# Kernel tuning notes

Measured on AMD Instinct MI355X. Metric: run time of the kernel, lower is better.

## Reference

```python
import jax, jax.numpy as jnp
import numpy as np

B, S, H, NCOL, NH = 32, 512, 768, 32, 12
HD = H // NH  # head dim 64
LN_EPS = 1e-12


def setup_inputs() -> dict:
    key = jax.random.key(0)
    ks = jax.random.split(key, 20)
    s = 0.02
    inp = {
        'hidden_states': jax.random.normal(ks[0], (B, S, H), jnp.float32),
        'column_embeddings': jax.random.normal(ks[1], (B, NCOL, H), jnp.float32),
        'column_categories': jax.random.randint(ks[2], (B, NCOL), 0, 2, jnp.int32),
        'value_mask': jax.random.randint(ks[3], (B, S), 0, NCOL + 1, jnp.int32),
        'Wd': jax.random.normal(ks[4], (H, H), jnp.float32) * s,
        'bd': jnp.zeros((H,), jnp.float32),
        'Wc': jax.random.normal(ks[5], (H, H), jnp.float32) * s,
        'bc': jnp.zeros((H,), jnp.float32),
        'Wq': jax.random.normal(ks[6], (H, H), jnp.float32) * s,
        'bq': jnp.zeros((H,), jnp.float32),
        'Wk': jax.random.normal(ks[7], (H, H), jnp.float32) * s,
        'bk': jnp.zeros((H,), jnp.float32),
        'Wv': jax.random.normal(ks[8], (H, H), jnp.float32) * s,
        'bv': jnp.zeros((H,), jnp.float32),
        'Wo': jax.random.normal(ks[9], (H, H), jnp.float32) * s,
        'bo': jnp.zeros((H,), jnp.float32),
        'ln_g': jnp.ones((H,), jnp.float32),
        'ln_b': jnp.zeros((H,), jnp.float32),
    }
    return inp


def _layernorm(x, g, b):
    mu = jnp.mean(x, axis=-1, keepdims=True)
    var = jnp.mean(jnp.square(x - mu), axis=-1, keepdims=True)
    return (x - mu) * jax.lax.rsqrt(var + LN_EPS) * g + b


def reference(hidden_states, column_embeddings, column_categories, value_mask,
              Wd, bd, Wc, bc, Wq, bq, Wk, bk, Wv, bv, Wo, bo, ln_g, ln_b):
    # dense branch
    h_ = hidden_states @ Wd.T + bd  # [B,S,H]
    # column gather: zero out category==0 columns, prepend zero row for index 0
    table = column_embeddings * (column_categories == 1)[..., None].astype(column_embeddings.dtype)
    table = jnp.concatenate([jnp.zeros_like(table[:, :1]), table], axis=1)  # [B,NCOL+1,H]
    h_col = jnp.take_along_axis(table, value_mask[..., None].astype(jnp.int32), axis=1)  # [B,S,H]
    h = jax.nn.gelu(h_ + (h_col @ Wc.T + bc), approximate=False)
    # Roberta self-attention
    def heads(x):
        return x.reshape(B, S, NH, HD).transpose(0, 2, 1, 3)  # [B,NH,S,HD]
    q = heads(h @ Wq.T + bq)
    k = heads(h @ Wk.T + bk)
    v = heads(h @ Wv.T + bv)
    scores = jnp.einsum('bhsd,bhtd->bhst', q, k) / jnp.sqrt(jnp.float32(HD))
    probs = jax.nn.softmax(scores, axis=-1)
    ctx = jnp.einsum('bhst,bhtd->bhsd', probs, v).transpose(0, 2, 1, 3).reshape(B, S, H)
    # self-output: dense + residual + layernorm
    out = _layernorm(ctx @ Wo.T + bo + h, ln_g, ln_b)
    return out
```

## Files before the change

kernel.cpp:

```cpp
#include <hip/hip_runtime.h>
#include <hip/hip_bf16.h>
#include <math.h>
#include <stdint.h>

#define B_    32
#define S_    512
#define H_    768
#define NH_   12
#define HD_   64
#define NCOL_ 32
#define M_    (B_*S_)

typedef __bf16 bf16;
typedef __bf16 bf16x8 __attribute__((ext_vector_type(8)));
typedef __bf16 bf16x4 __attribute__((ext_vector_type(4)));
typedef float  f32x4  __attribute__((ext_vector_type(4)));

__device__ __forceinline__ void async_load16(const void* g, void* l) {
    __builtin_amdgcn_global_load_lds(
        (__attribute__((address_space(1))) unsigned int*)g,
        (__attribute__((address_space(3))) unsigned int*)l, 16, 0, 0);
}

__device__ __forceinline__ bf16x8 cvt8(const float* p) {
    const float4* fp = (const float4*)p;
    float4 x = fp[0], y = fp[1];
    bf16x8 r;
    r[0] = (bf16)x.x; r[1] = (bf16)x.y; r[2] = (bf16)x.z; r[3] = (bf16)x.w;
    r[4] = (bf16)y.x; r[5] = (bf16)y.y; r[6] = (bf16)y.z; r[7] = (bf16)y.w;
    return r;
}

__global__ __launch_bounds__(256) void cvt_kernel(
    const float* __restrict__ hidden, const float* __restrict__ ce,
    const int* __restrict__ cc, const int* __restrict__ vm,
    const float* __restrict__ Wd, const float* __restrict__ Wc,
    const float* __restrict__ Wq, const float* __restrict__ Wk,
    const float* __restrict__ Wv, const float* __restrict__ Wo,
    const float* __restrict__ bq, const float* __restrict__ bk,
    const float* __restrict__ bv,
    bf16* __restrict__ hbf, bf16* __restrict__ hcol,
    bf16* __restrict__ wpack, float* __restrict__ bqkv)
{
    int blk = blockIdx.x;
    if (blk < 6144) {
        int id = blk * 256 + threadIdx.x;
        int row = id / 96, c = id - row * 96;
        *(bf16x8*)&hbf[(long)row * H_ + c * 8] = cvt8(hidden + (long)row * H_ + c * 8);
    } else if (blk < 12288) {
        int id = (blk - 6144) * 256 + threadIdx.x;
        int row = id / 96, c = id - row * 96;
        int b = row >> 9;
        int m = vm[row];
        bf16x8 val;
#pragma unroll
        for (int i = 0; i < 8; i++) val[i] = (bf16)0.0f;
        if (m > 0) {
            int col = m - 1;
            if (cc[b * NCOL_ + col] == 1)
                val = cvt8(ce + ((long)(b * NCOL_ + col)) * H_ + c * 8);
        }
        *(bf16x8*)&hcol[(long)row * H_ + c * 8] = val;
    } else {
        int id = (blk - 12288) * 256 + threadIdx.x;
        if (id < 442368) {
            const float* src;
            int r = id;
            if      (r < 73728)  { src = Wd; }
            else if (r < 147456) { src = Wc; r -= 73728; }
            else if (r < 221184) { src = Wq; r -= 147456; }
            else if (r < 294912) { src = Wk; r -= 221184; }
            else if (r < 368640) { src = Wv; r -= 294912; }
            else                 { src = Wo; r -= 368640; }
            *(bf16x8*)&wpack[(long)id * 8] = cvt8(src + (long)r * 8);
        } else if (id < 442656) {
            int j0 = (id - 442368) * 8;
#pragma unroll
            for (int i = 0; i < 8; i++) {
                int j = j0 + i;
                float v = (j < 768) ? bq[j] : (j < 1536) ? bk[j - 768] : bv[j - 1536];
                bqkv[j] = v;
            }
        }
    }
}

__global__ __launch_bounds__(512, 4) void gemm_qkv(
    const bf16* __restrict__ A, const bf16* __restrict__ Bw,
    const float* __restrict__ bias, bf16* __restrict__ out)
{
    __shared__ __align__(16) bf16 LB[36864];

    const int tid  = threadIdx.x;
    const int lane = tid & 63;
    const int wave = tid >> 6;
    const int wr   = wave >> 1;
    const int wc   = wave & 1;
    const int quad = lane >> 4;
    const int ln16 = lane & 15;

    const int bid = blockIdx.x;
    const int xcd = bid & 7;
    const int idx = bid >> 3;
    const int m0  = (xcd * 8 + (idx & 7)) * 256;
    const int n0  = (idx >> 3) * 128;

    int arow[2], acol[2];
#pragma unroll
    for (int q = 0; q < 2; q++) {
        int l = q * 512 + tid;
        int row = l >> 2;
        arow[q] = row;
        acol[q] = ((l & 3) ^ ((row >> 1) & 3)) * 8;
    }
    const int brow = tid >> 2;
    const int bcol = ((tid & 3) ^ ((brow >> 1) & 3)) * 8;

    auto stage = [&](int kt, int bsel) {
        int kk = kt * 32;
        const bf16* ag = A + kk;
        const bf16* bg = Bw + kk;
        bf16* SAb = &LB[bsel * 8192];
        bf16* SBb = &LB[24576 + bsel * 4096];
        async_load16(ag + (long)(m0 + arow[0]) * H_ + acol[0], SAb + tid * 8);
        async_load16(ag + (long)(m0 + arow[1]) * H_ + acol[1], SAb + 4096 + tid * 8);
        async_load16(bg + (long)(n0 + brow)    * H_ + bcol,    SBb + tid * 8);
    };

    f32x4 acc[4][4];
    const f32x4 zero4 = {0.f, 0.f, 0.f, 0.f};
#pragma unroll
    for (int i = 0; i < 4; i++)
#pragma unroll
        for (int j = 0; j < 4; j++) acc[i][j] = zero4;

    const int s4 = (ln16 >> 1) & 3;
    int aoff[4], boff[4];
#pragma unroll
    for (int i = 0; i < 4; i++) {
        aoff[i] = (wr * 64 + i * 16 + ln16) * 32 + (quad ^ s4) * 8;
        boff[i] = (wc * 64 + i * 16 + ln16) * 32 + (quad ^ s4) * 8;
    }

    const int nt = 24;

    stage(0, 0);
    stage(1, 1);
    asm volatile("s_waitcnt vmcnt(3)" ::: "memory");
    __builtin_amdgcn_sched_barrier(0);
    __builtin_amdgcn_s_barrier();

    int bs = 0;
    for (int t = 0; t < nt; ++t) {
        const int ps = (bs + 2 >= 3) ? bs - 1 : bs + 2;

        bf16x8 af[4], bfr[4];
#pragma unroll
        for (int i = 0; i < 4; i++) af[i]  = *(const bf16x8*)&LB[bs * 8192 + aoff[i]];
#pragma unroll
        for (int j = 0; j < 4; j++) bfr[j] = *(const bf16x8*)&LB[24576 + bs * 4096 + boff[j]];
        if (t + 2 < nt) stage(t + 2, ps);

        __builtin_amdgcn_s_setprio(1);
#pragma unroll
        for (int i = 0; i < 4; i++)
#pragma unroll
            for (int j = 0; j < 4; j++)
                acc[i][j] = __builtin_amdgcn_mfma_f32_16x16x32_bf16(af[i], bfr[j], acc[i][j], 0, 0, 0);
        __builtin_amdgcn_s_setprio(0);

        if (t + 2 < nt)       { asm volatile("s_waitcnt vmcnt(3)" ::: "memory"); }
        else if (t + 1 < nt)  { asm volatile("s_waitcnt vmcnt(0)" ::: "memory"); }
        __builtin_amdgcn_sched_barrier(0);
        if (t + 1 < nt) __builtin_amdgcn_s_barrier();
        bs = (bs + 1 == 3) ? 0 : bs + 1;
    }

    __syncthreads();
    bf16* scr = &LB[wave * 4608];

    const int cs0  = n0 + wc * 64;
    const int sec  = (cs0 >= 1536) ? 2 : ((cs0 >= 768) ? 1 : 0);
    const int head = (cs0 - sec * 768) >> 6;
    bf16* dst = out + (long)sec * M_ * H_;

#pragma unroll
    for (int j = 0; j < 4; j++) {
        const int d_loc = j * 16 + ln16;
        const float bj = bias[cs0 + d_loc];
#pragma unroll
        for (int i = 0; i < 4; i++) {
#pragma unroll
            for (int r = 0; r < 4; r++) {
                const int s_loc = i * 16 + quad * 4 + r;
                const float v = acc[i][j][r] + bj;
                scr[(sec == 2) ? (d_loc * 72 + s_loc) : (s_loc * 72 + d_loc)] = (bf16)v;
            }
        }
    }
    asm volatile("s_waitcnt lgkmcnt(0)" ::: "memory");
    __builtin_amdgcn_sched_barrier(0);

    const int g8 = lane >> 3;
    const int o8 = (lane & 7) * 8;
    if (sec < 2) {
#pragma unroll
        for (int it = 0; it < 8; it++) {
            const int s_loc = it * 8 + g8;
            const int row_s = m0 + wr * 64 + s_loc;
            const int b = row_s >> 9, s = row_s & 511;
            *(bf16x8*)&dst[(((long)(b * NH_ + head)) * S_ + s) * HD_ + o8] =
                *(const bf16x8*)&scr[s_loc * 72 + o8];
        }
    } else {
        const int row0 = m0 + wr * 64;
        const int b = row0 >> 9, sb = row0 & 511;
#pragma unroll
        for (int it = 0; it < 8; it++) {
            const int d_loc = it * 8 + g8;
            *(bf16x8*)&dst[(((long)(b * NH_ + head)) * HD_ + d_loc) * S_ + sb + o8] =
                *(const bf16x8*)&scr[d_loc * 72 + o8];
        }
    }
}

template<int MODE>
__global__ __launch_bounds__(256, 3) void gemm_bt(
    const bf16* __restrict__ A0, const bf16* __restrict__ A1,
    const bf16* __restrict__ B0, const bf16* __restrict__ B1,
    const float* __restrict__ bias1, const float* __restrict__ bias2,
    const bf16* __restrict__ resid, bf16* __restrict__ out,
    int K, int KSPLIT)
{
    __shared__ __align__(16) bf16 SA[3][128 * 32];
    __shared__ __align__(16) bf16 SB[3][128 * 32];

    const int tid  = threadIdx.x;
    const int lane = tid & 63;
    const int wave = tid >> 6;
    const int wr   = wave >> 1;
    const int wc   = wave & 1;
    const int quad = lane >> 4;
    const int ln16 = lane & 15;

    const int bid = blockIdx.x;
    const int xcd = bid & 7;
    const int idx = bid >> 3;
    const int m0  = (xcd * 16 + (idx & 15)) * 128;
    const int n0  = (idx >> 4) * 128;

    int arow[2], acol[2];
#pragma unroll
    for (int q = 0; q < 2; q++) {
        int l = q * 256 + tid;
        int row = l >> 2;
        arow[q] = row;
        acol[q] = ((l & 3) ^ ((row >> 1) & 3)) * 8;
    }

    auto stage = [&](int kt, int bsel) {
        int kk = kt * 32;
        const bf16* ag = (kk < KSPLIT) ? A0 + kk : A1 + (kk - KSPLIT);
        const bf16* bg = (kk < KSPLIT) ? B0 + kk : B1 + (kk - KSPLIT);
        async_load16(ag + (long)(m0 + arow[0]) * H_ + acol[0], &SA[bsel][tid * 8]);
        async_load16(ag + (long)(m0 + arow[1]) * H_ + acol[1], &SA[bsel][2048 + tid * 8]);
        async_load16(bg + (long)(n0 + arow[0]) * H_ + acol[0], &SB[bsel][tid * 8]);
        async_load16(bg + (long)(n0 + arow[1]) * H_ + acol[1], &SB[bsel][2048 + tid * 8]);
    };

    f32x4 acc[4][4];
    const f32x4 zero4 = {0.f, 0.f, 0.f, 0.f};
#pragma unroll
    for (int i = 0; i < 4; i++)
#pragma unroll
        for (int j = 0; j < 4; j++) acc[i][j] = zero4;

    const int s4 = (ln16 >> 1) & 3;
    int aoff[4], boff[4];
#pragma unroll
    for (int i = 0; i < 4; i++) {
        aoff[i] = (wr * 64 + i * 16 + ln16) * 32 + (quad ^ s4) * 8;
        boff[i] = (wc * 64 + i * 16 + ln16) * 32 + (quad ^ s4) * 8;
    }

    const int nt = K >> 5;

    stage(0, 0);
    stage(1, 1);
    asm volatile("s_waitcnt vmcnt(4)" ::: "memory");
    __builtin_amdgcn_sched_barrier(0);
    __builtin_amdgcn_s_barrier();

    int bs = 0;
    for (int t = 0; t < nt; ++t) {
        const int ps = (bs + 2 >= 3) ? bs - 1 : bs + 2;

        bf16x8 af[4], bfr[4];
#pragma unroll
        for (int i = 0; i < 4; i++) af[i]  = *(const bf16x8*)&SA[bs][aoff[i]];
#pragma unroll
        for (int j = 0; j < 4; j++) bfr[j] = *(const bf16x8*)&SB[bs][boff[j]];
        if (t + 2 < nt) stage(t + 2, ps);

        __builtin_amdgcn_s_setprio(1);
#pragma unroll
        for (int i = 0; i < 4; i++)
#pragma unroll
            for (int j = 0; j < 4; j++)
                acc[i][j] = __builtin_amdgcn_mfma_f32_16x16x32_bf16(af[i], bfr[j], acc[i][j], 0, 0, 0);
        __builtin_amdgcn_s_setprio(0);

        if (t + 2 < nt)       { asm volatile("s_waitcnt vmcnt(4)" ::: "memory"); }
        else if (t + 1 < nt)  { asm volatile("s_waitcnt vmcnt(0)" ::: "memory"); }
        __builtin_amdgcn_sched_barrier(0);
        if (t + 1 < nt) __builtin_amdgcn_s_barrier();
        bs = (bs + 1 == 3) ? 0 : bs + 1;
    }

    const int c_r = quad * 4;
    const int c_c = ln16;

#pragma unroll
    for (int j = 0; j < 4; j++) {
        const int col = n0 + wc * 64 + j * 16 + c_c;
        float bias = bias1[col];
        if (MODE == 0) bias += bias2[col];
#pragma unroll
        for (int i = 0; i < 4; i++) {
#pragma unroll
            for (int r = 0; r < 4; r++) {
                const int row = m0 + wr * 64 + i * 16 + c_r + r;
                float v = acc[i][j][r] + bias;
                if (MODE == 0) {
                    v = 0.5f * v * (1.0f + erff(v * 0.70710678118654752f));
                    out[(long)row * H_ + col] = (bf16)v;
                } else {
                    v += (float)resid[(long)row * H_ + col];
                    out[(long)row * H_ + col] = (bf16)v;
                }
            }
        }
    }
}

#define QP 72

__global__ __launch_bounds__(256) void attn_kernel(
    const bf16* __restrict__ q, const bf16* __restrict__ k,
    const bf16* __restrict__ vt, bf16* __restrict__ ctx)
{
    __shared__ __align__(16) bf16 Qs[64 * QP];
    __shared__ __align__(16) bf16 Ks[64 * QP];
    __shared__ __align__(16) bf16 Vt[64 * QP];
    __shared__ __align__(16) bf16 Ps[4][16 * QP];

    const int tid  = threadIdx.x;
    const int lane = tid & 63;
    const int w    = tid >> 6;
    const int quad = lane >> 4;
    const int ln16 = lane & 15;

    const int bid = blockIdx.x;
    const int qt  = bid / 384;
    const int g   = bid - qt * 384;
    const int b   = g / 12;
    const int h   = g - b * 12;
    const long base = ((long)(b * NH_ + h)) * S_ * HD_;

    const int r0 = tid >> 2;
    const int e0 = (tid & 3) * 16;

    {
        const bf16* qg = q + base + (long)qt * 64 * HD_;
        *(uint4*)&Qs[r0 * QP + e0]     = *(const uint4*)&qg[r0 * HD_ + e0];
        *(uint4*)&Qs[r0 * QP + e0 + 8] = *(const uint4*)&qg[r0 * HD_ + e0 + 8];
    }
    const bf16* kg = k  + base;
    const bf16* vg = vt + base;
    uint4 kr0 = *(const uint4*)&kg[r0 * HD_ + e0];
    uint4 kr1 = *(const uint4*)&kg[r0 * HD_ + e0 + 8];
    uint4 vr0 = *(const uint4*)&vg[(long)r0 * S_ + e0];
    uint4 vr1 = *(const uint4*)&vg[(long)r0 * S_ + e0 + 8];
    __syncthreads();

    const bf16x8 bq0 = *(const bf16x8*)&Qs[(w * 16 + ln16) * QP + quad * 8];
    const bf16x8 bq1 = *(const bf16x8*)&Qs[(w * 16 + ln16) * QP + 32 + quad * 8];

    f32x4 O[4];
    const f32x4 zero4 = {0.f, 0.f, 0.f, 0.f};
#pragma unroll
    for (int t = 0; t < 4; t++) O[t] = zero4;
    float mo = -1e30f, l = 0.f;

    const float SCL = 0.18033688011112042f;

    for (int kc = 0; kc < 8; kc++) {
        __syncthreads();
        *(uint4*)&Ks[r0 * QP + e0]     = kr0;
        *(uint4*)&Ks[r0 * QP + e0 + 8] = kr1;
        *(uint4*)&Vt[r0 * QP + e0]     = vr0;
        *(uint4*)&Vt[r0 * QP + e0 + 8] = vr1;
        {
            int kcn = (kc < 7) ? kc + 1 : 7;
            kr0 = *(const uint4*)&kg[(long)kcn * 64 * HD_ + r0 * HD_ + e0];
            kr1 = *(const uint4*)&kg[(long)kcn * 64 * HD_ + r0 * HD_ + e0 + 8];
            vr0 = *(const uint4*)&vg[(long)r0 * S_ + kcn * 64 + e0];
            vr1 = *(const uint4*)&vg[(long)r0 * S_ + kcn * 64 + e0 + 8];
        }
        __syncthreads();

        f32x4 sc[4];
#pragma unroll
        for (int i = 0; i < 4; i++) {
            bf16x8 a0 = *(const bf16x8*)&Ks[(i * 16 + ln16) * QP + quad * 8];
            bf16x8 a1 = *(const bf16x8*)&Ks[(i * 16 + ln16) * QP + 32 + quad * 8];
            sc[i] = zero4;
            sc[i] = __builtin_amdgcn_mfma_f32_16x16x32_bf16(a0, bq0, sc[i], 0, 0, 0);
            sc[i] = __builtin_amdgcn_mfma_f32_16x16x32_bf16(a1, bq1, sc[i], 0, 0, 0);
        }

        float cm = -1e30f;
#pragma unroll
        for (int i = 0; i < 4; i++)
#pragma unroll
            for (int r = 0; r < 4; r++) {
                float s = sc[i][r] * SCL;
                sc[i][r] = s;
                cm = fmaxf(cm, s);
            }
        cm = fmaxf(cm, __shfl_xor(cm, 16));
        cm = fmaxf(cm, __shfl_xor(cm, 32));

        if (!__all(cm - mo <= 8.0f)) {
            float mn = fmaxf(mo, cm);
            float alpha = exp2f(mo - mn);
            l *= alpha;
#pragma unroll
            for (int t = 0; t < 4; t++)
#pragma unroll
                for (int r = 0; r < 4; r++) O[t][r] *= alpha;
            mo = mn;
        }

        float rs = 0.f;
#pragma unroll
        for (int i = 0; i < 4; i++) {
            bf16x4 pk;
#pragma unroll
            for (int r = 0; r < 4; r++) {
                float p = exp2f(sc[i][r] - mo);
                rs += p;
                pk[r] = (bf16)p;
            }
            *(bf16x4*)&Ps[w][ln16 * QP + i * 16 + quad * 4] = pk;
        }
        rs += __shfl_xor(rs, 16);
        rs += __shfl_xor(rs, 32);
        l  += rs;

        bf16x8 bp0 = *(const bf16x8*)&Ps[w][ln16 * QP + quad * 8];
        bf16x8 bp1 = *(const bf16x8*)&Ps[w][ln16 * QP + 32 + quad * 8];
#pragma unroll
        for (int dt = 0; dt < 4; dt++) {
            bf16x8 a0 = *(const bf16x8*)&Vt[(dt * 16 + ln16) * QP + quad * 8];
            bf16x8 a1 = *(const bf16x8*)&Vt[(dt * 16 + ln16) * QP + 32 + quad * 8];
            O[dt] = __builtin_amdgcn_mfma_f32_16x16x32_bf16(a0, bp0, O[dt], 0, 0, 0);
            O[dt] = __builtin_amdgcn_mfma_f32_16x16x32_bf16(a1, bp1, O[dt], 0, 0, 0);
        }
    }

    {
        float inv = 1.0f / l;
#pragma unroll
        for (int dt = 0; dt < 4; dt++) {
            bf16x4 ov;
#pragma unroll
            for (int r = 0; r < 4; r++) ov[r] = (bf16)(O[dt][r] * inv);
            *(bf16x4*)&Qs[(w * 16 + ln16) * QP + dt * 16 + quad * 4] = ov;
        }
    }
    __syncthreads();
    {
        uint4 o0 = *(const uint4*)&Qs[r0 * QP + e0];
        uint4 o1 = *(const uint4*)&Qs[r0 * QP + e0 + 8];
        bf16* cg = ctx + ((long)(b * S_ + qt * 64 + r0)) * H_ + h * HD_;
        *(uint4*)&cg[e0]     = o0;
        *(uint4*)&cg[e0 + 8] = o1;
    }
}

__global__ __launch_bounds__(256) void ln_kernel(
    const bf16* __restrict__ y, const float* __restrict__ g,
    const float* __restrict__ be, float* __restrict__ out)
{
    const int lane = threadIdx.x & 63;
    const int w    = threadIdx.x >> 6;
    const long row = (long)blockIdx.x * 4 + w;
    const bf16* yr = y + row * H_;

    float x[12];
    float sum = 0.f, ss = 0.f;
#pragma unroll
    for (int j = 0; j < 12; j++) {
        x[j] = (float)yr[j * 64 + lane];
        sum += x[j];
        ss  += x[j] * x[j];
    }
#pragma unroll
    for (int m = 1; m < 64; m <<= 1) {
        sum += __shfl_xor(sum, m);
        ss  += __shfl_xor(ss, m);
    }
    const float mu  = sum * (1.0f / 768.0f);
    float var = ss * (1.0f / 768.0f) - mu * mu;
    const float rs = rsqrtf(fmaxf(var, 0.f) + 1e-12f);
#pragma unroll
    for (int j = 0; j < 12; j++) {
        int c = j * 64 + lane;
        out[row * H_ + c] = (x[j] - mu) * rs * g[c] + be[c];
    }
}

extern "C" void kernel_launch(void* const* d_in, const int* in_sizes, int n_in,
                              void* d_out, int out_size, void* d_ws, size_t ws_size,
                              hipStream_t stream)
{
    const float* hidden = (const float*)d_in[0];
    const float* ce     = (const float*)d_in[1];
    const int*   cc     = (const int*)d_in[2];
    const int*   vm     = (const int*)d_in[3];
    const float* Wd     = (const float*)d_in[4];
    const float* bd     = (const float*)d_in[5];
    const float* Wc     = (const float*)d_in[6];
    const float* bc     = (const float*)d_in[7];
    const float* Wq     = (const float*)d_in[8];
    const float* bq     = (const float*)d_in[9];
    const float* Wk     = (const float*)d_in[10];
    const float* bk     = (const float*)d_in[11];
    const float* Wv     = (const float*)d_in[12];
    const float* bv     = (const float*)d_in[13];
    const float* Wo     = (const float*)d_in[14];
    const float* bo     = (const float*)d_in[15];
    const float* lng    = (const float*)d_in[16];
    const float* lnb    = (const float*)d_in[17];

    const long NE = (long)M_ * H_;
    bf16* ws   = (bf16*)d_ws;
    bf16* hbuf = ws;
    bf16* qkv  = ws + NE;
    bf16* hbf  = qkv;
    bf16* hcol = qkv + NE;
    bf16* qb   = qkv;
    bf16* kb   = qkv + NE;
    bf16* vb   = qkv + 2 * NE;
    bf16* wpack = ws + 4 * NE;
    const bf16* Wd_b  = wpack;
    const bf16* Wc_b  = wpack + 589824;
    const bf16* Wq_b  = wpack + 1179648;
    const bf16* Wo_b  = wpack + 2949120;
    float* bqkv = (float*)(wpack + 3538944);
    bf16* ctx = (bf16*)d_out;

    cvt_kernel<<<14018, 256, 0, stream>>>(hidden, ce, cc, vm, Wd, Wc, Wq, Wk, Wv, Wo,
                                          bq, bk, bv, hbf, hcol, wpack, bqkv);

    gemm_bt<0><<<768, 256, 0, stream>>>(hbf, hcol, Wd_b, Wc_b, bd, bc, nullptr, hbuf, 2 * H_, H_);
    gemm_qkv<<<1152, 512, 0, stream>>>(hbuf, Wq_b, bqkv, qkv);
    attn_kernel<<<3072, 256, 0, stream>>>(qb, kb, vb, ctx);
    gemm_bt<2><<<768, 256, 0, stream>>>(ctx, ctx, Wo_b, Wo_b, bo, nullptr, hbuf, hbuf, H_, H_);
    ln_kernel<<<M_ / 4, 256, 0, stream>>>(hbuf, lng, lnb, (float*)d_out);
}
```

Baseline: 369.4 us.

## Shrink LDS to double buffering and raise occupancy in QKV and dense GEMMs

Both GEMM kernels drop from a 3-stage to a 2-stage LDS ring, adding an extra barrier after the fragment reads so the next stage can safely overwrite the current buffer. The smaller LDS footprint and raised launch bounds are meant to let more blocks share a CU and hide memory latency through occupancy instead of deeper prefetch. The QKV epilogue is split into two halves with a smaller scratch area, including a packed transposed write for V, and the XCD-aware block swizzle is replaced by a plain linear mapping. In exchange, each iteration gains a barrier and has less prefetch slack, and the higher occupancy targets may squeeze registers and cause spills.

```diff
diff --git a/kernel.cpp b/kernel.cpp
--- a/kernel.cpp
+++ b/kernel.cpp
@@ -85,11 +85,11 @@
     }
 }
 
-__global__ __launch_bounds__(512, 4) void gemm_qkv(
+__global__ __launch_bounds__(512, 6) void gemm_qkv(
     const bf16* __restrict__ A, const bf16* __restrict__ Bw,
     const float* __restrict__ bias, bf16* __restrict__ out)
 {
-    __shared__ __align__(16) bf16 LB[36864];
+    __shared__ __align__(16) bf16 LB[24576];
 
     const int tid  = threadIdx.x;
     const int lane = tid & 63;
@@ -100,10 +100,8 @@
     const int ln16 = lane & 15;
 
     const int bid = blockIdx.x;
-    const int xcd = bid & 7;
-    const int idx = bid >> 3;
-    const int m0  = (xcd * 8 + (idx & 7)) * 256;
-    const int n0  = (idx >> 3) * 128;
+    const int m0  = (bid & 63) * 256;
+    const int n0  = (bid >> 6) * 128;
 
     int arow[2], acol[2];
 #pragma unroll
@@ -121,7 +119,7 @@
         const bf16* ag = A + kk;
         const bf16* bg = Bw + kk;
         bf16* SAb = &LB[bsel * 8192];
-        bf16* SBb = &LB[24576 + bsel * 4096];
+        bf16* SBb = &LB[16384 + bsel * 4096];
         async_load16(ag + (long)(m0 + arow[0]) * H_ + acol[0], SAb + tid * 8);
         async_load16(ag + (long)(m0 + arow[1]) * H_ + acol[1], SAb + 4096 + tid * 8);
         async_load16(bg + (long)(n0 + brow)    * H_ + bcol,    SBb + tid * 8);
@@ -150,16 +148,18 @@
     __builtin_amdgcn_sched_barrier(0);
     __builtin_amdgcn_s_barrier();
 
-    int bs = 0;
     for (int t = 0; t < nt; ++t) {
-        const int ps = (bs + 2 >= 3) ? bs - 1 : bs + 2;
+        const int bs = t & 1;
 
         bf16x8 af[4], bfr[4];
 #pragma unroll
         for (int i = 0; i < 4; i++) af[i]  = *(const bf16x8*)&LB[bs * 8192 + aoff[i]];
 #pragma unroll
-        for (int j = 0; j < 4; j++) bfr[j] = *(const bf16x8*)&LB[24576 + bs * 4096 + boff[j]];
-        if (t + 2 < nt) stage(t + 2, ps);
+        for (int j = 0; j < 4; j++) bfr[j] = *(const bf16x8*)&LB[16384 + bs * 4096 + boff[j]];
+        asm volatile("s_waitcnt lgkmcnt(0)" ::: "memory");
+        __builtin_amdgcn_sched_barrier(0);
+        __builtin_amdgcn_s_barrier();
+        if (t + 2 < nt) stage(t + 2, bs);
 
         __builtin_amdgcn_s_setprio(1);
 #pragma unroll
@@ -173,67 +173,80 @@
         else if (t + 1 < nt)  { asm volatile("s_waitcnt vmcnt(0)" ::: "memory"); }
         __builtin_amdgcn_sched_barrier(0);
         if (t + 1 < nt) __builtin_amdgcn_s_barrier();
-        bs = (bs + 1 == 3) ? 0 : bs + 1;
     }
 
     __syncthreads();
-    bf16* scr = &LB[wave * 4608];
+    bf16* scr = &LB[wave * 3072];
 
     const int cs0  = n0 + wc * 64;
     const int sec  = (cs0 >= 1536) ? 2 : ((cs0 >= 768) ? 1 : 0);
     const int head = (cs0 - sec * 768) >> 6;
     bf16* dst = out + (long)sec * M_ * H_;
 
-#pragma unroll
-    for (int j = 0; j < 4; j++) {
-        const int d_loc = j * 16 + ln16;
-        const float bj = bias[cs0 + d_loc];
-#pragma unroll
-        for (int i = 0; i < 4; i++) {
-#pragma unroll
-            for (int r = 0; r < 4; r++) {
-                const int s_loc = i * 16 + quad * 4 + r;
-                const float v = acc[i][j][r] + bj;
-                scr[(sec == 2) ? (d_loc * 72 + s_loc) : (s_loc * 72 + d_loc)] = (bf16)v;
-            }
-        }
-    }
-    asm volatile("s_waitcnt lgkmcnt(0)" ::: "memory");
-    __builtin_amdgcn_sched_barrier(0);
-
-    const int g8 = lane >> 3;
-    const int o8 = (lane & 7) * 8;
     if (sec < 2) {
-#pragma unroll
-        for (int it = 0; it < 8; it++) {
-            const int s_loc = it * 8 + g8;
-            const int row_s = m0 + wr * 64 + s_loc;
-            const int b = row_s >> 9, s = row_s & 511;
-            *(bf16x8*)&dst[(((long)(b * NH_ + head)) * S_ + s) * HD_ + o8] =
-                *(const bf16x8*)&scr[s_loc * 72 + o8];
+        const int g8 = lane >> 3, o8 = (lane & 7) * 8;
+#pragma unroll
+        for (int h = 0; h < 2; h++) {
+#pragma unroll
+            for (int j = 0; j < 4; j++) {
+                const int d_loc = j * 16 + ln16;
+                const float bj = bias[cs0 + d_loc];
+#pragma unroll
+                for (int i2 = 0; i2 < 2; i2++)
+#pragma unroll
+                    for (int r = 0; r < 4; r++) {
+                        const int s_rel = i2 * 16 + quad * 4 + r;
+                        scr[s_rel * 72 + d_loc] = (bf16)(acc[h * 2 + i2][j][r] + bj);
+                    }
+            }
+#pragma unroll
+            for (int it = 0; it < 4; it++) {
+                const int s_rel = it * 8 + g8;
+                const int row_s = m0 + wr * 64 + h * 32 + s_rel;
+                const int b = row_s >> 9, s = row_s & 511;
+                *(bf16x8*)&dst[(((long)(b * NH_ + head)) * S_ + s) * HD_ + o8] =
+                    *(const bf16x8*)&scr[s_rel * 72 + o8];
+            }
         }
     } else {
+        const int l4 = lane >> 2, o4 = (lane & 3) * 8;
         const int row0 = m0 + wr * 64;
-        const int b = row0 >> 9, sb = row0 & 511;
-#pragma unroll
-        for (int it = 0; it < 8; it++) {
-            const int d_loc = it * 8 + g8;
-            *(bf16x8*)&dst[(((long)(b * NH_ + head)) * HD_ + d_loc) * S_ + sb + o8] =
-                *(const bf16x8*)&scr[d_loc * 72 + o8];
+        const int b = row0 >> 9;
+#pragma unroll
+        for (int h = 0; h < 2; h++) {
+#pragma unroll
+            for (int j = 0; j < 4; j++) {
+                const int d_loc = j * 16 + ln16;
+                const float bj = bias[cs0 + d_loc];
+#pragma unroll
+                for (int i2 = 0; i2 < 2; i2++) {
+                    bf16x4 pk;
+#pragma unroll
+                    for (int r = 0; r < 4; r++) pk[r] = (bf16)(acc[h * 2 + i2][j][r] + bj);
+                    *(bf16x4*)&scr[d_loc * 40 + i2 * 16 + quad * 4] = pk;
+                }
+            }
+            const int sb = (row0 & 511) + h * 32;
+#pragma unroll
+            for (int it = 0; it < 4; it++) {
+                const int d_loc = it * 16 + l4;
+                *(bf16x8*)&dst[(((long)(b * NH_ + head)) * HD_ + d_loc) * S_ + sb + o4] =
+                    *(const bf16x8*)&scr[d_loc * 40 + o4];
+            }
         }
     }
 }
 
 template<int MODE>
-__global__ __launch_bounds__(256, 3) void gemm_bt(
+__global__ __launch_bounds__(256, 5) void gemm_bt(
     const bf16* __restrict__ A0, const bf16* __restrict__ A1,
     const bf16* __restrict__ B0, const bf16* __restrict__ B1,
     const float* __restrict__ bias1, const float* __restrict__ bias2,
     const bf16* __restrict__ resid, bf16* __restrict__ out,
     int K, int KSPLIT)
 {
-    __shared__ __align__(16) bf16 SA[3][128 * 32];
-    __shared__ __align__(16) bf16 SB[3][128 * 32];
+    __shared__ __align__(16) bf16 SA[2][128 * 32];
+    __shared__ __align__(16) bf16 SB[2][128 * 32];
 
     const int tid  = threadIdx.x;
     const int lane = tid & 63;
@@ -291,16 +304,18 @@
     __builtin_amdgcn_sched_barrier(0);
     __builtin_amdgcn_s_barrier();
 
-    int bs = 0;
     for (int t = 0; t < nt; ++t) {
-        const int ps = (bs + 2 >= 3) ? bs - 1 : bs + 2;
+        const int bs = t & 1;
 
         bf16x8 af[4], bfr[4];
 #pragma unroll
         for (int i = 0; i < 4; i++) af[i]  = *(const bf16x8*)&SA[bs][aoff[i]];
 #pragma unroll
         for (int j = 0; j < 4; j++) bfr[j] = *(const bf16x8*)&SB[bs][boff[j]];
-        if (t + 2 < nt) stage(t + 2, ps);
+        asm volatile("s_waitcnt lgkmcnt(0)" ::: "memory");
+        __builtin_amdgcn_sched_barrier(0);
+        __builtin_amdgcn_s_barrier();
+        if (t + 2 < nt) stage(t + 2, bs);
 
         __builtin_amdgcn_s_setprio(1);
 #pragma unroll
@@ -314,7 +329,6 @@
         else if (t + 1 < nt)  { asm volatile("s_waitcnt vmcnt(0)" ::: "memory"); }
         __builtin_amdgcn_sched_barrier(0);
         if (t + 1 < nt) __builtin_amdgcn_s_barrier();
-        bs = (bs + 1 == 3) ? 0 : bs + 1;
     }
 
     const int c_r = quad * 4;
```

New measurement: 1.021 ms. 2.77x slower.
